# Kernel optimization log

Measured on AMD Instinct MI355X. Metric: run time of the kernel, lower is better.

The kernel has to match this reference:

```python
import jax, jax.numpy as jnp
import numpy as np

D_HIDDEN = 1024
N_HEADS = 16
D_HEAD = 64
B, N = 4, 1024
EPS = 1e-5


def _lin(x, w, b):
    # torch Linear: y = x @ W^T + b, w: [out, in]
    return jnp.einsum('...i,oi->...o', x, w) + b


def _ln(x, g, b):
    m = jnp.mean(x, axis=-1, keepdims=True)
    v = jnp.mean(jnp.square(x - m), axis=-1, keepdims=True)
    return (x - m) * jax.lax.rsqrt(v + EPS) * g + b


def setup_inputs() -> dict:
    key = jax.random.key(0)
    ks = jax.random.split(key, 20)
    d = D_HIDDEN
    s = 0.02
    inp = {
        'x': jax.random.normal(ks[0], (B, N, d), jnp.float32),
        'time_emb': jax.random.normal(ks[1], (B, d), jnp.float32),
        'ln1_g': jnp.ones((d,), jnp.float32),
        'ln1_b': jnp.zeros((d,), jnp.float32),
        's1_w': jax.random.normal(ks[2], (d, d), jnp.float32) * s,
        's1_b': jnp.zeros((d,), jnp.float32),
        'o1_w': jax.random.normal(ks[3], (d, d), jnp.float32) * s,
        'o1_b': jnp.zeros((d,), jnp.float32),
        'qkv_w': jax.random.normal(ks[4], (3 * d, d), jnp.float32) * s,
        'qkv_b': jnp.zeros((3 * d,), jnp.float32),
        'proj_w': jax.random.normal(ks[5], (d, d), jnp.float32) * s,
        'proj_b': jnp.zeros((d,), jnp.float32),
        'ln2_g': jnp.ones((d,), jnp.float32),
        'ln2_b': jnp.zeros((d,), jnp.float32),
        's2_w': jax.random.normal(ks[6], (d, d), jnp.float32) * s,
        's2_b': jnp.zeros((d,), jnp.float32),
        'o2_w': jax.random.normal(ks[7], (d, d), jnp.float32) * s,
        'o2_b': jnp.zeros((d,), jnp.float32),
        'up_w': jax.random.normal(ks[8], (4 * d, d), jnp.float32) * s,
        'up_b': jnp.zeros((4 * d,), jnp.float32),
        'down_w': jax.random.normal(ks[9], (d, 4 * d), jnp.float32) * s,
        'down_b': jnp.zeros((d,), jnp.float32),
    }
    return inp


def reference(x, time_emb, ln1_g, ln1_b, s1_w, s1_b, o1_w, o1_b,
              qkv_w, qkv_b, proj_w, proj_b, ln2_g, ln2_b,
              s2_w, s2_b, o2_w, o2_b, up_w, up_b, down_w, down_b):
    d = D_HIDDEN

    def ada(h, sw, sb, ow, ob):
        scale = _lin(time_emb, sw, sb)[:, None, :]   # [B,1,d]
        offset = _lin(time_emb, ow, ob)[:, None, :]
        return (1.0 + scale) * h + offset

    # attention branch
    h = ada(_ln(x, ln1_g, ln1_b), s1_w, s1_b, o1_w, o1_b)
    qkv = _lin(h, qkv_w, qkv_b)                       # [B,N,3d]
    q, k, v = jnp.split(qkv, 3, axis=-1)
    q = q.reshape(B, N, N_HEADS, D_HEAD)
    k = k.reshape(B, N, N_HEADS, D_HEAD)
    v = v.reshape(B, N, N_HEADS, D_HEAD)
    wei = jnp.einsum('bnhd,bmhd->bhnm', q, k) * (D_HEAD ** -0.5)
    wei = jax.nn.softmax(wei, axis=-1)
    attn = jnp.einsum('bhnm,bmhd->bnhd', wei, v).reshape(B, N, d)
    x = x + _lin(attn, proj_w, proj_b)

    # mlp branch (torch nn.GELU default = exact erf gelu)
    h = ada(_ln(x, ln2_g, ln2_b), s2_w, s2_b, o2_w, o2_b)
    h = jax.nn.gelu(_lin(h, up_w, up_b), approximate=False)
    x = x + _lin(h, down_w, down_b)
    return x, time_emb
```

## Files before the change

kernel.cpp:

```cpp
#include <hip/hip_runtime.h>
#include <hip/hip_bf16.h>
#include <math.h>

#define DH 1024
#define BB 4
#define NN 1024
#define NH 16
#define HD 64

typedef __attribute__((ext_vector_type(8))) short bf16x8;
typedef __attribute__((ext_vector_type(4))) float f32x4;
typedef unsigned short u16;

static __device__ __forceinline__ u16 f2bf(float f) {
  __hip_bfloat16 h = __float2bfloat16(f);
  return *reinterpret_cast<u16*>(&h);
}

#define MFMA16(a, b, c) __builtin_amdgcn_mfma_f32_16x16x32_bf16(a, b, c, 0, 0, 0)
#define VMCNT(n) asm volatile("s_waitcnt vmcnt(" #n ")" ::: "memory")
#define MEMFENCE asm volatile("" ::: "memory")

static __device__ __forceinline__ void async16(const void* g, void* l) {
  __builtin_amdgcn_global_load_lds(
      (const __attribute__((address_space(1))) void*)g,
      (__attribute__((address_space(3))) void*)l, 16, 0, 0);
}

__global__ void cvt_all_kernel(const float* __restrict__ wq, const float* __restrict__ wp,
                               const float* __restrict__ wu, const float* __restrict__ wd,
                               u16* __restrict__ oq, u16* __restrict__ op,
                               u16* __restrict__ ou, u16* __restrict__ od) {
  int i = blockIdx.x * 256 + threadIdx.x;
  const float* src; u16* dst; int off;
  if (i < 786432)            { src = wq; dst = oq; off = i; }
  else if (i < 1048576)      { src = wp; dst = op; off = i - 786432; }
  else if (i < 2097152)      { src = wu; dst = ou; off = i - 1048576; }
  else                       { src = wd; dst = od; off = i - 2097152; }
  float4 v = reinterpret_cast<const float4*>(src)[off];
  ushort4 o;
  o.x = f2bf(v.x); o.y = f2bf(v.y); o.z = f2bf(v.z); o.w = f2bf(v.w);
  reinterpret_cast<ushort4*>(dst)[off] = o;
}

__global__ __launch_bounds__(256) void adaln_kernel(
    const float* __restrict__ e,
    const float* __restrict__ w_s1, const float* __restrict__ b_s1,
    const float* __restrict__ w_o1, const float* __restrict__ b_o1,
    const float* __restrict__ w_s2, const float* __restrict__ b_s2,
    const float* __restrict__ w_o2, const float* __restrict__ b_o2,
    float* __restrict__ out) {
  int tid = threadIdx.x, wid = tid >> 6, lane = tid & 63;
  int mat = blockIdx.y;
  const float* w; const float* bs; float addc;
  if (mat == 0)      { w = w_s1; bs = b_s1; addc = 1.f; }
  else if (mat == 1) { w = w_o1; bs = b_o1; addc = 0.f; }
  else if (mat == 2) { w = w_s2; bs = b_s2; addc = 1.f; }
  else               { w = w_o2; bs = b_o2; addc = 0.f; }
  int col = blockIdx.x * 4 + wid;
  float a0 = 0.f, a1 = 0.f, a2 = 0.f, a3 = 0.f;
  const float* wc_ = w + (size_t)col * DH;
  for (int i = 0; i < 16; ++i) {
    int k = i * 64 + lane;
    float wv = wc_[k];
    a0 += wv * e[k];
    a1 += wv * e[DH + k];
    a2 += wv * e[2 * DH + k];
    a3 += wv * e[3 * DH + k];
  }
  #pragma unroll
  for (int msk = 32; msk; msk >>= 1) {
    a0 += __shfl_xor(a0, msk); a1 += __shfl_xor(a1, msk);
    a2 += __shfl_xor(a2, msk); a3 += __shfl_xor(a3, msk);
  }
  if (lane == 0) {
    float bb = bs[col] + addc;
    out[mat * (4 * DH) + 0 * DH + col] = a0 + bb;
    out[mat * (4 * DH) + 1 * DH + col] = a1 + bb;
    out[mat * (4 * DH) + 2 * DH + col] = a2 + bb;
    out[mat * (4 * DH) + 3 * DH + col] = a3 + bb;
  }
}

__global__ __launch_bounds__(256) void ln_mod_kernel(
    const float* __restrict__ x, const float* __restrict__ g, const float* __restrict__ bta,
    const float* __restrict__ sp, const float* __restrict__ off, u16* __restrict__ out) {
  int row = blockIdx.x;
  int b = row >> 10;
  int tid = threadIdx.x;
  int wid = tid >> 6, lane = tid & 63;
  const float4 xv = reinterpret_cast<const float4*>(x + (size_t)row * DH)[tid];
  float s = xv.x + xv.y + xv.z + xv.w;
  float ss = xv.x * xv.x + xv.y * xv.y + xv.z * xv.z + xv.w * xv.w;
  #pragma unroll
  for (int m = 32; m; m >>= 1) { s += __shfl_xor(s, m); ss += __shfl_xor(ss, m); }
  __shared__ float red[8];
  if (lane == 0) { red[wid] = s; red[4 + wid] = ss; }
  __syncthreads();
  s = red[0] + red[1] + red[2] + red[3];
  ss = red[4] + red[5] + red[6] + red[7];
  float mean = s * (1.f / DH);
  float var = ss * (1.f / DH) - mean * mean;
  float rstd = rsqrtf(var + 1e-5f);
  int c = tid * 4;
  const float* spb = sp + b * DH + c;
  const float* offb = off + b * DH + c;
  float y0 = (xv.x - mean) * rstd * g[c + 0] + bta[c + 0];
  float y1 = (xv.y - mean) * rstd * g[c + 1] + bta[c + 1];
  float y2 = (xv.z - mean) * rstd * g[c + 2] + bta[c + 2];
  float y3 = (xv.w - mean) * rstd * g[c + 3] + bta[c + 3];
  ushort4 o;
  o.x = f2bf(spb[0] * y0 + offb[0]);
  o.y = f2bf(spb[1] * y1 + offb[1]);
  o.z = f2bf(spb[2] * y2 + offb[2]);
  o.w = f2bf(spb[3] * y3 + offb[3]);
  reinterpret_cast<ushort4*>(out + (size_t)row * DH)[tid] = o;
}

enum { EPI_BF16 = 0, EPI_GELU = 1, EPI_F32PART = 2 };

template <int EPI>
__global__ __launch_bounds__(512, 2) void gemm256_kernel(
    const u16* __restrict__ A, const u16* __restrict__ W,
    const float* __restrict__ bias, void* __restrict__ outp,
    int N, int K, int KT) {
  extern __shared__ u16 lds[];
  u16* Ab = lds;
  u16* Bb = lds + 32768;
  int tid = threadIdx.x;
  int wid = tid >> 6, lane = tid & 63;
  int l15 = lane & 15, l4 = lane >> 4;
  int wr = wid >> 2, wc = wid & 3;

  int nwg = gridDim.x * gridDim.y;
  int lin = blockIdx.y * gridDim.x + blockIdx.x;
  int q8 = nwg >> 3;
  int lin2 = (lin & 7) * q8 + (lin >> 3);
  int bx = lin2 % gridDim.x, by = lin2 / gridDim.x;
  int m0 = by * 256, n0 = bx * 256;
  int k0 = blockIdx.z * (KT << 5);

  f32x4 acc[8][4] = {};

  const u16* Abase = A + (size_t)m0 * K + k0;
  const u16* Wbase = W + (size_t)n0 * K + k0;
  int i0 = tid, i1 = 512 + tid;
  int r0 = i0 >> 2, c0 = (i0 & 3) ^ ((r0 >> 1) & 3);
  int r1 = i1 >> 2, c1 = (i1 & 3) ^ ((r1 >> 1) & 3);
  size_t gO0 = (size_t)r0 * K + c0 * 8;
  size_t gO1 = (size_t)r1 * K + c1 * 8;
  int lb0 = (wid * 64) * 8;
  int lb1 = (512 + wid * 64) * 8;

  auto stage = [&](int tt) {
    int q = (tt & 3) * 8192;
    const u16* Ak = Abase + tt * 32;
    const u16* Wk = Wbase + tt * 32;
    async16(Ak + gO0, &Ab[q + lb0]);
    async16(Ak + gO1, &Ab[q + lb1]);
    async16(Wk + gO0, &Bb[q + lb0]);
    async16(Wk + gO1, &Bb[q + lb1]);
  };

  auto compute = [&](int tt) {
    int q = (tt & 3) * 8192;
    bf16x8 af[8], bfr[4];
    #pragma unroll
    for (int m = 0; m < 8; ++m) {
      int row = wr * 128 + m * 16 + l15;
      int ps = l4 ^ ((row >> 1) & 3);
      af[m] = *reinterpret_cast<const bf16x8*>(&Ab[q + row * 32 + ps * 8]);
    }
    #pragma unroll
    for (int n = 0; n < 4; ++n) {
      int row = wc * 64 + n * 16 + l15;
      int ps = l4 ^ ((row >> 1) & 3);
      bfr[n] = *reinterpret_cast<const bf16x8*>(&Bb[q + row * 32 + ps * 8]);
    }
    #pragma unroll
    for (int m = 0; m < 8; ++m)
      #pragma unroll
      for (int n = 0; n < 4; ++n)
        acc[m][n] = MFMA16(af[m], bfr[n], acc[m][n]);
  };

  stage(0);
  if (KT > 1) stage(1);
  if (KT > 2) stage(2);
  for (int t = 0; t < KT; ++t) {
    if (t < KT - 3) { stage(t + 3); VMCNT(12); }
    else if (t == KT - 3) { VMCNT(8); }
    else if (t == KT - 2) { VMCNT(4); }
    else { VMCNT(0); }
    __builtin_amdgcn_s_barrier();
    MEMFENCE;
    compute(t);
    MEMFENCE;
    __builtin_amdgcn_s_barrier();
  }

  int M = gridDim.y * 256;
  float* fout = (float*)outp + (size_t)blockIdx.z * M * N;
  #pragma unroll
  for (int n = 0; n < 4; ++n) {
    int col = n0 + wc * 64 + n * 16 + l15;
    float bv = (EPI == EPI_F32PART) ? 0.f : bias[col];
    #pragma unroll
    for (int m = 0; m < 8; ++m) {
      #pragma unroll
      for (int r = 0; r < 4; ++r) {
        int rowg = m0 + wr * 128 + m * 16 + l4 * 4 + r;
        float v = acc[m][n][r] + bv;
        if (EPI == EPI_GELU) {
          v = 0.5f * v * (1.f + erff(v * 0.70710678118f));
          ((u16*)outp)[(size_t)rowg * N + col] = f2bf(v);
        } else if (EPI == EPI_BF16) {
          ((u16*)outp)[(size_t)rowg * N + col] = f2bf(v);
        } else {
          fout[(size_t)rowg * N + col] = v;
        }
      }
    }
  }
}

enum { OEPI_BF16 = 0, OEPI_GELU = 1, OEPI_RES = 2 };

template <int EPI>
__global__ __launch_bounds__(256, 3) void gemm_bt_kernel(
    const u16* __restrict__ A, const u16* __restrict__ W,
    const float* __restrict__ bias, const float* __restrict__ resid,
    void* __restrict__ outp, int N, int K) {
  __shared__ __align__(16) u16 As[2][128 * 32];
  __shared__ __align__(16) u16 Ws[2][128 * 32];
  int tid = threadIdx.x;
  int wid = tid >> 6, lane = tid & 63;
  int l15 = lane & 15, l4 = lane >> 4;
  int m0 = blockIdx.y * 128, n0 = blockIdx.x * 128;
  int wr = wid >> 1, wc = wid & 1;
  f32x4 acc[4][4] = {};

  const int KT = K >> 5;
  int idx0 = tid, idx1 = 256 + tid;
  int rowA0 = idx0 >> 2, gs0 = (idx0 & 3) ^ ((rowA0 >> 1) & 3);
  int rowA1 = idx1 >> 2, gs1 = (idx1 & 3) ^ ((rowA1 >> 1) & 3);
  const u16* Abase = A + (size_t)m0 * K;
  const u16* Wbase = W + (size_t)n0 * K;
  int lb0 = (wid * 64) * 8;
  int lb1 = (256 + wid * 64) * 8;

  auto stage = [&](int buf, int kt) {
    const u16* Ak = Abase + kt * 32;
    const u16* Wk = Wbase + kt * 32;
    async16(Ak + (size_t)rowA0 * K + gs0 * 8, &As[buf][lb0]);
    async16(Wk + (size_t)rowA0 * K + gs0 * 8, &Ws[buf][lb0]);
    async16(Ak + (size_t)rowA1 * K + gs1 * 8, &As[buf][lb1]);
    async16(Wk + (size_t)rowA1 * K + gs1 * 8, &Ws[buf][lb1]);
  };

  auto compute = [&](int buf) {
    bf16x8 af[4], wf[4];
    #pragma unroll
    for (int m = 0; m < 4; ++m) {
      int row = wr * 64 + m * 16 + l15;
      int ps = l4 ^ ((row >> 1) & 3);
      af[m] = *reinterpret_cast<const bf16x8*>(&As[buf][row * 32 + ps * 8]);
    }
    #pragma unroll
    for (int n = 0; n < 4; ++n) {
      int row = wc * 64 + n * 16 + l15;
      int ps = l4 ^ ((row >> 1) & 3);
      wf[n] = *reinterpret_cast<const bf16x8*>(&Ws[buf][row * 32 + ps * 8]);
    }
    #pragma unroll
    for (int m = 0; m < 4; ++m)
      #pragma unroll
      for (int n = 0; n < 4; ++n)
        acc[m][n] = MFMA16(af[m], wf[n], acc[m][n]);
  };

  stage(0, 0);
  __syncthreads();
  int buf = 0;
  for (int kt = 0; kt < KT - 1; ++kt) {
    stage(buf ^ 1, kt + 1);
    compute(buf);
    __syncthreads();
    buf ^= 1;
  }
  compute(buf);

  #pragma unroll
  for (int n = 0; n < 4; ++n) {
    int col = n0 + wc * 64 + n * 16 + l15;
    float bv = bias[col];
    #pragma unroll
    for (int m = 0; m < 4; ++m) {
      #pragma unroll
      for (int r = 0; r < 4; ++r) {
        int rowg = m0 + wr * 64 + m * 16 + l4 * 4 + r;
        float v = acc[m][n][r] + bv;
        if (EPI == OEPI_GELU) {
          v = 0.5f * v * (1.f + erff(v * 0.70710678118f));
          ((u16*)outp)[(size_t)rowg * N + col] = f2bf(v);
        } else if (EPI == OEPI_BF16) {
          ((u16*)outp)[(size_t)rowg * N + col] = f2bf(v);
        } else {
          ((float*)outp)[(size_t)rowg * N + col] = v + resid[(size_t)rowg * N + col];
        }
      }
    }
  }
}

__global__ __launch_bounds__(256) void reduce4_kernel(
    const float* __restrict__ part, const float* __restrict__ x2,
    const float* __restrict__ bias, const float* __restrict__ te,
    float* __restrict__ out) {
  size_t i = (size_t)blockIdx.x * 256 + threadIdx.x;
  const size_t MN4 = (size_t)4096 * 1024 / 4;
  float4 a0 = reinterpret_cast<const float4*>(part)[i];
  float4 a1 = reinterpret_cast<const float4*>(part)[i + MN4];
  float4 a2 = reinterpret_cast<const float4*>(part)[i + 2 * MN4];
  float4 a3 = reinterpret_cast<const float4*>(part)[i + 3 * MN4];
  float4 xr = reinterpret_cast<const float4*>(x2)[i];
  int col = (int)((i * 4) & 1023);
  float4 bv = *reinterpret_cast<const float4*>(&bias[col]);
  float4 o;
  o.x = xr.x + bv.x + a0.x + a1.x + a2.x + a3.x;
  o.y = xr.y + bv.y + a0.y + a1.y + a2.y + a3.y;
  o.z = xr.z + bv.z + a0.z + a1.z + a2.z + a3.z;
  o.w = xr.w + bv.w + a0.w + a1.w + a2.w + a3.w;
  reinterpret_cast<float4*>(out)[i] = o;
  if (blockIdx.x < 16) {
    int ii = blockIdx.x * 256 + threadIdx.x;
    out[4096 * 1024 + ii] = te[ii];
  }
}

__global__ __launch_bounds__(256) void vt_kernel(const u16* __restrict__ qkvb,
                                                 u16* __restrict__ vT) {
  __shared__ u16 L[64 * 66];
  int bh = blockIdx.y;
  int b = bh >> 4, h = bh & 15;
  int nt = blockIdx.x;
  int t = threadIdx.x;
  const u16* src = qkvb + ((size_t)b * 1024 + nt * 64) * 3072 + 2048 + h * 64;
  int j = t >> 3, s = t & 7;
  bf16x8 r0 = *reinterpret_cast<const bf16x8*>(src + (size_t)j * 3072 + s * 8);
  bf16x8 r1 = *reinterpret_cast<const bf16x8*>(src + (size_t)(j + 32) * 3072 + s * 8);
  #pragma unroll
  for (int e = 0; e < 8; ++e) {
    L[(s * 8 + e) * 66 + j] = r0[e];
    L[(s * 8 + e) * 66 + j + 32] = r1[e];
  }
  __syncthreads();
  int d = t & 63, cp = t >> 6;
  u16* dst = vT + ((size_t)bh * 64 + d) * 1024 + nt * 64;
  #pragma unroll
  for (int half = 0; half < 2; ++half) {
    int cs = cp + half * 4;
    bf16x8 o;
    #pragma unroll
    for (int c = 0; c < 8; ++c) o[c] = L[d * 66 + cs * 8 + c];
    *reinterpret_cast<bf16x8*>(dst + cs * 8) = o;
  }
}

__global__ __launch_bounds__(256, 4) void attn_kernel(
    const u16* __restrict__ qkv, const u16* __restrict__ vT, u16* __restrict__ out) {
  __shared__ __align__(16) u16 Ks[2][4096];
  __shared__ __align__(16) u16 Vs[2][4096];
  __shared__ __align__(16) u16 Ps[4][1024];
  int tid = threadIdx.x, wid = tid >> 6, lane = tid & 63;
  int l15 = lane & 15, l4 = lane >> 4;
  int L = blockIdx.y * gridDim.x + blockIdx.x;
  int qt = (L >> 3) & 15;
  int bh = (L & 7) | ((L >> 7) << 3);
  int b = bh >> 4, h = bh & 15;
  const size_t SN = 3 * DH;
  const u16* qb = qkv + (size_t)b * NN * SN + h * HD;
  const u16* kb = qb + DH;
  const u16* vtb = vT + (size_t)bh * 64 * 1024;

  int qrow = qt * 64 + wid * 16 + l15;
  bf16x8 qf[2];
  #pragma unroll
  for (int ks = 0; ks < 2; ++ks)
    qf[ks] = *reinterpret_cast<const bf16x8*>(qb + (size_t)qrow * SN + ks * 32 + l4 * 8);

  float m_[4], l_[4];
  f32x4 o_[4] = {};
  #pragma unroll
  for (int r = 0; r < 4; ++r) { m_[r] = -1e30f; l_[r] = 0.f; }

  int iA = tid, iB = 256 + tid;
  int jA = iA >> 3, sA = iA & 7, gsA = sA ^ (jA & 7);
  int jB = iB >> 3, sB = iB & 7, gsB = sB ^ (jB & 7);

  auto stageKV = [&](int bufn, int t) {
    const u16* kt = kb + (size_t)t * 64 * SN;
    async16(kt + (size_t)jA * SN + gsA * 8, &Ks[bufn][iA * 8]);
    async16(kt + (size_t)jB * SN + gsB * 8, &Ks[bufn][iB * 8]);
    const u16* vt = vtb + (size_t)t * 64;
    async16(vt + (size_t)jA * 1024 + gsA * 8, &Vs[bufn][iA * 8]);
    async16(vt + (size_t)jB * 1024 + gsB * 8, &Vs[bufn][iB * 8]);
  };

  stageKV(0, 0);
  __syncthreads();

  int buf = 0;
  for (int t = 0; t < 16; ++t) {
    if (t < 15) stageKV(buf ^ 1, t + 1);

    f32x4 sa[4];
    #pragma unroll
    for (int nb = 0; nb < 4; ++nb) {
      f32x4 s = {};
      #pragma unroll
      for (int ks = 0; ks < 2; ++ks) {
        int j = nb * 16 + l15;
        int ps = (ks * 4 + l4) ^ (j & 7);
        bf16x8 kf = *reinterpret_cast<const bf16x8*>(&Ks[buf][j * 64 + ps * 8]);
        s = MFMA16(qf[ks], kf, s);
      }
      sa[nb] = s * 0.125f;
    }

    float rm[4], tsum[4];
    #pragma unroll
    for (int r = 0; r < 4; ++r) {
      float v = fmaxf(fmaxf(sa[0][r], sa[1][r]), fmaxf(sa[2][r], sa[3][r]));
      #pragma unroll
      for (int msk = 1; msk < 16; msk <<= 1) v = fmaxf(v, __shfl_xor(v, msk));
      rm[r] = v;
    }
    float gmx = fmaxf(fmaxf(rm[0] - m_[0], rm[1] - m_[1]),
                      fmaxf(rm[2] - m_[2], rm[3] - m_[3]));
    if (!__all(gmx <= 8.f)) {
      #pragma unroll
      for (int r = 0; r < 4; ++r) {
        float mn = fmaxf(m_[r], rm[r]);
        float corr = __expf(m_[r] - mn);
        m_[r] = mn;
        l_[r] *= corr;
        #pragma unroll
        for (int nd = 0; nd < 4; ++nd) o_[nd][r] *= corr;
      }
    }
    #pragma unroll
    for (int r = 0; r < 4; ++r) tsum[r] = 0.f;
    #pragma unroll
    for (int nb = 0; nb < 4; ++nb) {
      #pragma unroll
      for (int r = 0; r < 4; ++r) {
        float p = __expf(sa[nb][r] - m_[r]);
        sa[nb][r] = p;
        tsum[r] += p;
      }
    }
    #pragma unroll
    for (int r = 0; r < 4; ++r) {
      float v = tsum[r];
      #pragma unroll
      for (int msk = 1; msk < 16; msk <<= 1) v += __shfl_xor(v, msk);
      l_[r] += v;
    }

    u16* Pw = Ps[wid];
    #pragma unroll
    for (int nb = 0; nb < 4; ++nb) {
      int slot = nb * 2 + (l15 >> 3);
      #pragma unroll
      for (int r = 0; r < 4; ++r) {
        int row = l4 * 4 + r;
        int ps = slot ^ (row & 7);
        Pw[row * 64 + ps * 8 + (l15 & 7)] = f2bf(sa[nb][r]);
      }
    }

    __builtin_amdgcn_s_setprio(1);
    #pragma unroll
    for (int ks = 0; ks < 2; ++ks) {
      int psp = (ks * 4 + l4) ^ (l15 & 7);
      bf16x8 pa = *reinterpret_cast<const bf16x8*>(&Pw[l15 * 64 + psp * 8]);
      #pragma unroll
      for (int nd = 0; nd < 4; ++nd) {
        int d = nd * 16 + l15;
        int psv = (ks * 4 + l4) ^ (d & 7);
        bf16x8 vf = *reinterpret_cast<const bf16x8*>(&Vs[buf][d * 64 + psv * 8]);
        o_[nd] = MFMA16(pa, vf, o_[nd]);
      }
    }
    __builtin_amdgcn_s_setprio(0);

    if (t < 15) __syncthreads();
    buf ^= 1;
  }

  float inv[4];
  #pragma unroll
  for (int r = 0; r < 4; ++r) inv[r] = 1.f / l_[r];
  u16* ob = out + (size_t)b * NN * DH + h * HD;
  #pragma unroll
  for (int nd = 0; nd < 4; ++nd) {
    #pragma unroll
    for (int r = 0; r < 4; ++r) {
      int q = qt * 64 + wid * 16 + l4 * 4 + r;
      ob[(size_t)q * DH + nd * 16 + l15] = f2bf(o_[nd][r] * inv[r]);
    }
  }
}

extern "C" void kernel_launch(void* const* d_in, const int* in_sizes, int n_in,
                              void* d_out, int out_size, void* d_ws, size_t ws_size,
                              hipStream_t stream) {
  (void)in_sizes; (void)n_in; (void)out_size; (void)ws_size;
  const float* x      = (const float*)d_in[0];
  const float* te     = (const float*)d_in[1];
  const float* ln1_g  = (const float*)d_in[2];
  const float* ln1_b  = (const float*)d_in[3];
  const float* s1_w   = (const float*)d_in[4];
  const float* s1_b   = (const float*)d_in[5];
  const float* o1_w   = (const float*)d_in[6];
  const float* o1_b   = (const float*)d_in[7];
  const float* qkv_w  = (const float*)d_in[8];
  const float* qkv_b  = (const float*)d_in[9];
  const float* proj_w = (const float*)d_in[10];
  const float* proj_b = (const float*)d_in[11];
  const float* ln2_g  = (const float*)d_in[12];
  const float* ln2_b  = (const float*)d_in[13];
  const float* s2_w   = (const float*)d_in[14];
  const float* s2_b   = (const float*)d_in[15];
  const float* o2_w   = (const float*)d_in[16];
  const float* o2_b   = (const float*)d_in[17];
  const float* up_w   = (const float*)d_in[18];
  const float* up_b   = (const float*)d_in[19];
  const float* down_w = (const float*)d_in[20];
  const float* down_b = (const float*)d_in[21];

  char* ws = (char*)d_ws;
  size_t off = 0;
  auto alloc = [&](size_t bytes) { void* p = ws + off; off += (bytes + 255) & ~255ull; return p; };
  u16*   wq   = (u16*)  alloc((size_t)3072 * 1024 * 2);
  u16*   wp   = (u16*)  alloc((size_t)1024 * 1024 * 2);
  u16*   wu   = (u16*)  alloc((size_t)4096 * 1024 * 2);
  u16*   h1   = (u16*)  alloc((size_t)4096 * 1024 * 2);
  u16*   qkvb = (u16*)  alloc((size_t)4096 * 3072 * 2);
  u16*   att  = (u16*)  alloc((size_t)4096 * 1024 * 2);
  u16*   h2   = (u16*)  alloc((size_t)4096 * 1024 * 2);
  u16*   wd   = (u16*)  alloc((size_t)1024 * 4096 * 2);
  float* x2   = (float*)alloc((size_t)4096 * 1024 * 4);
  u16*   upb  = (u16*)  alloc((size_t)4096 * 4096 * 2);
  float* ada  = (float*)alloc((size_t)4 * 4 * 1024 * 4);
  float* sp1 = ada, *off1 = ada + 4096, *sp2 = ada + 8192, *off2 = ada + 12288;
  float* part = (float*)wq;
  u16*   vT   = h1;

  cvt_all_kernel<<<12288, 256, 0, stream>>>(qkv_w, proj_w, up_w, down_w, wq, wp, wu, wd);
  adaln_kernel<<<dim3(256, 4), 256, 0, stream>>>(te, s1_w, s1_b, o1_w, o1_b, s2_w, s2_b, o2_w, o2_b, ada);
  ln_mod_kernel<<<4096, 256, 0, stream>>>(x, ln1_g, ln1_b, sp1, off1, h1);
  gemm256_kernel<EPI_BF16><<<dim3(12, 16, 1), 512, 131072, stream>>>(h1, wq, qkv_b, qkvb, 3072, 1024, 32);
  vt_kernel<<<dim3(16, 64), 256, 0, stream>>>(qkvb, vT);
  attn_kernel<<<dim3(16, 64), 256, 0, stream>>>(qkvb, vT, att);
  gemm_bt_kernel<OEPI_RES><<<dim3(8, 32), 256, 0, stream>>>(att, wp, proj_b, x, x2, 1024, 1024);
  ln_mod_kernel<<<4096, 256, 0, stream>>>(x2, ln2_g, ln2_b, sp2, off2, h2);
  gemm256_kernel<EPI_GELU><<<dim3(16, 16, 1), 512, 131072, stream>>>(h2, wu, up_b, upb, 4096, 1024, 32);
  gemm256_kernel<EPI_F32PART><<<dim3(4, 16, 4), 512, 131072, stream>>>(upb, wd, nullptr, part, 1024, 4096, 32);
  reduce4_kernel<<<4096, 256, 0, stream>>>(part, x2, down_b, te, (float*)d_out);
}
```

Baseline: 274.1 us.

## Halve GEMM LDS pipeline to double buffering and store split-K partials in bf16

```diff
diff --git a/kernel.cpp b/kernel.cpp
--- a/kernel.cpp
+++ b/kernel.cpp
@@ -15,6 +15,9 @@
 static __device__ __forceinline__ u16 f2bf(float f) {
   __hip_bfloat16 h = __float2bfloat16(f);
   return *reinterpret_cast<u16*>(&h);
+}
+static __device__ __forceinline__ float bf2f(u16 x) {
+  return __uint_as_float((unsigned)x << 16);
 }
 
 #define MFMA16(a, b, c) __builtin_amdgcn_mfma_f32_16x16x32_bf16(a, b, c, 0, 0, 0)
@@ -117,16 +120,16 @@
   reinterpret_cast<ushort4*>(out + (size_t)row * DH)[tid] = o;
 }
 
-enum { EPI_BF16 = 0, EPI_GELU = 1, EPI_F32PART = 2 };
+enum { EPI_BF16 = 0, EPI_GELU = 1, EPI_PART = 2 };
 
 template <int EPI>
-__global__ __launch_bounds__(512, 2) void gemm256_kernel(
+__global__ __launch_bounds__(512, 4) void gemm256_kernel(
     const u16* __restrict__ A, const u16* __restrict__ W,
     const float* __restrict__ bias, void* __restrict__ outp,
     int N, int K, int KT) {
   extern __shared__ u16 lds[];
   u16* Ab = lds;
-  u16* Bb = lds + 32768;
+  u16* Bb = lds + 16384;
   int tid = threadIdx.x;
   int wid = tid >> 6, lane = tid & 63;
   int l15 = lane & 15, l4 = lane >> 4;
@@ -153,7 +156,7 @@
   int lb1 = (512 + wid * 64) * 8;
 
   auto stage = [&](int tt) {
-    int q = (tt & 3) * 8192;
+    int q = (tt & 1) * 8192;
     const u16* Ak = Abase + tt * 32;
     const u16* Wk = Wbase + tt * 32;
     async16(Ak + gO0, &Ab[q + lb0]);
@@ -163,7 +166,7 @@
   };
 
   auto compute = [&](int tt) {
-    int q = (tt & 3) * 8192;
+    int q = (tt & 1) * 8192;
     bf16x8 af[8], bfr[4];
     #pragma unroll
     for (int m = 0; m < 8; ++m) {
@@ -185,12 +188,8 @@
   };
 
   stage(0);
-  if (KT > 1) stage(1);
-  if (KT > 2) stage(2);
   for (int t = 0; t < KT; ++t) {
-    if (t < KT - 3) { stage(t + 3); VMCNT(12); }
-    else if (t == KT - 3) { VMCNT(8); }
-    else if (t == KT - 2) { VMCNT(4); }
+    if (t < KT - 1) { stage(t + 1); VMCNT(4); }
     else { VMCNT(0); }
     __builtin_amdgcn_s_barrier();
     MEMFENCE;
@@ -200,11 +199,11 @@
   }
 
   int M = gridDim.y * 256;
-  float* fout = (float*)outp + (size_t)blockIdx.z * M * N;
+  u16* pout = (u16*)outp + (size_t)blockIdx.z * M * N;
   #pragma unroll
   for (int n = 0; n < 4; ++n) {
     int col = n0 + wc * 64 + n * 16 + l15;
-    float bv = (EPI == EPI_F32PART) ? 0.f : bias[col];
+    float bv = (EPI == EPI_PART) ? 0.f : bias[col];
     #pragma unroll
     for (int m = 0; m < 8; ++m) {
       #pragma unroll
@@ -217,7 +216,7 @@
         } else if (EPI == EPI_BF16) {
           ((u16*)outp)[(size_t)rowg * N + col] = f2bf(v);
         } else {
-          fout[(size_t)rowg * N + col] = v;
+          pout[(size_t)rowg * N + col] = f2bf(v);
         }
       }
     }
@@ -314,23 +313,21 @@
 }
 
 __global__ __launch_bounds__(256) void reduce4_kernel(
-    const float* __restrict__ part, const float* __restrict__ x2,
+    const u16* __restrict__ part, const float* __restrict__ x2,
     const float* __restrict__ bias, const float* __restrict__ te,
     float* __restrict__ out) {
   size_t i = (size_t)blockIdx.x * 256 + threadIdx.x;
-  const size_t MN4 = (size_t)4096 * 1024 / 4;
-  float4 a0 = reinterpret_cast<const float4*>(part)[i];
-  float4 a1 = reinterpret_cast<const float4*>(part)[i + MN4];
-  float4 a2 = reinterpret_cast<const float4*>(part)[i + 2 * MN4];
-  float4 a3 = reinterpret_cast<const float4*>(part)[i + 3 * MN4];
+  const size_t MN = (size_t)4096 * 1024;
   float4 xr = reinterpret_cast<const float4*>(x2)[i];
   int col = (int)((i * 4) & 1023);
   float4 bv = *reinterpret_cast<const float4*>(&bias[col]);
-  float4 o;
-  o.x = xr.x + bv.x + a0.x + a1.x + a2.x + a3.x;
-  o.y = xr.y + bv.y + a0.y + a1.y + a2.y + a3.y;
-  o.z = xr.z + bv.z + a0.z + a1.z + a2.z + a3.z;
-  o.w = xr.w + bv.w + a0.w + a1.w + a2.w + a3.w;
+  float a0 = xr.x + bv.x, a1 = xr.y + bv.y, a2 = xr.z + bv.z, a3 = xr.w + bv.w;
+  #pragma unroll
+  for (int p = 0; p < 4; ++p) {
+    ushort4 u = reinterpret_cast<const ushort4*>(part + p * MN)[i];
+    a0 += bf2f(u.x); a1 += bf2f(u.y); a2 += bf2f(u.z); a3 += bf2f(u.w);
+  }
+  float4 o; o.x = a0; o.y = a1; o.z = a2; o.w = a3;
   reinterpret_cast<float4*>(out)[i] = o;
   if (blockIdx.x < 16) {
     int ii = blockIdx.x * 256 + threadIdx.x;
@@ -555,18 +552,18 @@
   u16*   upb  = (u16*)  alloc((size_t)4096 * 4096 * 2);
   float* ada  = (float*)alloc((size_t)4 * 4 * 1024 * 4);
   float* sp1 = ada, *off1 = ada + 4096, *sp2 = ada + 8192, *off2 = ada + 12288;
-  float* part = (float*)wq;
+  u16*   part = wq;
   u16*   vT   = h1;
 
   cvt_all_kernel<<<12288, 256, 0, stream>>>(qkv_w, proj_w, up_w, down_w, wq, wp, wu, wd);
   adaln_kernel<<<dim3(256, 4), 256, 0, stream>>>(te, s1_w, s1_b, o1_w, o1_b, s2_w, s2_b, o2_w, o2_b, ada);
   ln_mod_kernel<<<4096, 256, 0, stream>>>(x, ln1_g, ln1_b, sp1, off1, h1);
-  gemm256_kernel<EPI_BF16><<<dim3(12, 16, 1), 512, 131072, stream>>>(h1, wq, qkv_b, qkvb, 3072, 1024, 32);
+  gemm256_kernel<EPI_BF16><<<dim3(12, 16, 1), 512, 65536, stream>>>(h1, wq, qkv_b, qkvb, 3072, 1024, 32);
   vt_kernel<<<dim3(16, 64), 256, 0, stream>>>(qkvb, vT);
   attn_kernel<<<dim3(16, 64), 256, 0, stream>>>(qkvb, vT, att);
   gemm_bt_kernel<OEPI_RES><<<dim3(8, 32), 256, 0, stream>>>(att, wp, proj_b, x, x2, 1024, 1024);
   ln_mod_kernel<<<4096, 256, 0, stream>>>(x2, ln2_g, ln2_b, sp2, off2, h2);
-  gemm256_kernel<EPI_GELU><<<dim3(16, 16, 1), 512, 131072, stream>>>(h2, wu, up_b, upb, 4096, 1024, 32);
-  gemm256_kernel<EPI_F32PART><<<dim3(4, 16, 4), 512, 131072, stream>>>(upb, wd, nullptr, part, 1024, 4096, 32);
+  gemm256_kernel<EPI_GELU><<<dim3(16, 16, 1), 512, 65536, stream>>>(h2, wu, up_b, upb, 4096, 1024, 32);
+  gemm256_kernel<EPI_PART><<<dim3(4, 16, 4), 512, 65536, stream>>>(upb, wd, nullptr, part, 1024, 4096, 32);
   reduce4_kernel<<<4096, 256, 0, stream>>>(part, x2, down_b, te, (float*)d_out);
 }
```

New measurement: 623.8 us. +127.6%, slower.
